# Kernel optimization log

Measured on AMD Instinct MI355X. Metric: run time of the kernel, lower is better.

Reference implementation:

```python
import jax, jax.numpy as jnp
import numpy as np

K_CHUNK = 512  # key-chunk size used by the module when n > 5000


def setup_inputs() -> dict:
    key = jax.random.key(0)
    ks = jax.random.split(key, 9)
    b, n, d = 1, 8192, 512
    s = 1.0 / np.sqrt(d)
    x = jax.random.normal(ks[0], (b, n, d), dtype=jnp.float32)
    Wq = jax.random.normal(ks[1], (d, d), dtype=jnp.float32) * s
    bq = jax.random.normal(ks[2], (d,), dtype=jnp.float32) * 0.01
    Wk = jax.random.normal(ks[3], (d, d), dtype=jnp.float32) * s
    bk = jax.random.normal(ks[4], (d,), dtype=jnp.float32) * 0.01
    Wv = jax.random.normal(ks[5], (d, d), dtype=jnp.float32) * s
    bv = jax.random.normal(ks[6], (d,), dtype=jnp.float32) * 0.01
    Wo = jax.random.normal(ks[7], (d, d), dtype=jnp.float32) * s
    bo = jax.random.normal(ks[8], (d,), dtype=jnp.float32) * 0.01
    return {"x": x, "Wq": Wq, "bq": bq, "Wk": Wk, "bk": bk,
            "Wv": Wv, "bv": bv, "Wo": Wo, "bo": bo}


def reference(x, Wq, bq, Wk, bk, Wv, bv, Wo, bo):
    # Faithful to the n > 5000 branch of SimpleAttenLayer (eval mode: dropout = identity).
    # The q-chunking in the original does not change the math (each q row is independent),
    # so we vectorize over all queries. The k-chunking DOES change the math: softmax is
    # applied within each 512-wide key block, then a second softmax over the concatenated
    # per-block weights, then matmul with full v.
    b, n, d = x.shape
    assert n % K_CHUNK == 0
    q = x @ Wq + bq
    k = x @ Wk + bk
    v = x @ Wv + bv
    scores = jnp.einsum('bnd,bmd->bnm', q, k) / jnp.sqrt(jnp.float32(d))
    # softmax within each key chunk of size K_CHUNK
    w1 = jax.nn.softmax(scores.reshape(b, n, n // K_CHUNK, K_CHUNK), axis=-1)
    w1 = w1.reshape(b, n, n)
    # second (global) softmax over the concatenated chunk weights
    w2 = jax.nn.softmax(w1, axis=-1)
    attn_out = jnp.einsum('bnm,bmd->bnd', w2, v)
    cls_attn_weights = w2[:, 0:1, :]  # [b, 1, n]
    out = x + (attn_out @ Wo + bo)
    return (out, cls_attn_weights)
```

## Files before the change

### kernel.cpp

```cpp
#include <hip/hip_runtime.h>
#include <stdint.h>

typedef unsigned short u16;
typedef uint8_t u8;
typedef __bf16 bf16x8 __attribute__((ext_vector_type(8)));
typedef float f32x4 __attribute__((ext_vector_type(4)));
typedef long i64x2 __attribute__((ext_vector_type(2)));

#define NTOK 8192
#define DD 512
#define CHK 512
#define NCH 16
#define LOG2E 1.4426950408889634f
#define SCL 0.044194173824159216f
#define SCLL 0.063762069130835270f

__device__ __forceinline__ u16 f2bf(float f) {
  union { float f; uint32_t u; } v; v.f = f;
  uint32_t r = v.u + 0x7FFFu + ((v.u >> 16) & 1u);
  return (u16)(r >> 16);
}

template <int CTRL>
__device__ __forceinline__ float dppadd(float x) {
  int y = __builtin_amdgcn_update_dpp(0, __float_as_int(x), CTRL, 0xF, 0xF, true);
  return x + __int_as_float(y);
}
__device__ __forceinline__ float rowsum16(float x) {
  x = dppadd<0xB1>(x);
  x = dppadd<0x4E>(x);
  x = dppadd<0x141>(x);
  x = dppadd<0x140>(x);
  return x;
}

typedef const __attribute__((address_space(1))) unsigned int* gas_t;
typedef __attribute__((address_space(3))) unsigned int* las_t;
__device__ __forceinline__ void gload16(const void* g, void* l) {
  __builtin_amdgcn_global_load_lds((gas_t)g, (las_t)l, 16, 0, 0);
}

__device__ __forceinline__ void vm4bar() {
  asm volatile("s_waitcnt vmcnt(4)\n\ts_barrier" ::: "memory");
}
__device__ __forceinline__ void vm2bar() {
  asm volatile("s_waitcnt vmcnt(2)\n\ts_barrier" ::: "memory");
}
__device__ __forceinline__ void vm0bar() {
  asm volatile("s_waitcnt vmcnt(0)\n\ts_barrier" ::: "memory");
}
__device__ __forceinline__ void barx() {
  asm volatile("s_barrier" ::: "memory");
}
__device__ __forceinline__ void lgkm0() {
  asm volatile("s_waitcnt lgkmcnt(0)" ::: "memory");
  __builtin_amdgcn_sched_barrier(0);
}

__device__ __forceinline__ int ilv64(int p) {
  const int g = p >> 3;
  return (((g & 3) * 2) + (g >> 2)) * 8 + (p & 7);
}
__device__ __forceinline__ int fperm(int t) {
  const int p = ((t & 15) << 2) | ((t >> 4) & 3);
  return (t & ~63) | ilv64(p);
}

__global__ void prep_kernel(const float* __restrict__ x, const float* __restrict__ Wq,
                            const float* __restrict__ Wk, const float* __restrict__ Wv,
                            const float* __restrict__ Wo, const float* __restrict__ bq,
                            u16* __restrict__ xb, u16* __restrict__ Wall, u16* __restrict__ WoT,
                            float* __restrict__ lsum, float* __restrict__ q0g) {
  __shared__ float t[32][33];
  const int bid = blockIdx.x;
  const int tid = threadIdx.x;
  if (bid < 4096) {
    int i = bid * 256 + tid;
    if (bid < 32) lsum[bid * 256 + tid] = 0.f;
    float4 v = ((const float4*)x)[i];
    ushort4 o;
    o.x = f2bf(v.x); o.y = f2bf(v.y); o.z = f2bf(v.z); o.w = f2bf(v.w);
    ((ushort4*)xb)[i] = o;
  } else if (bid < 5120) {
    const int tt = bid - 4096;
    const int z = tt >> 8, idx = tt & 255;
    const float* W; u16* WT;
    if (z == 0)      { W = Wq; WT = Wall; }
    else if (z == 1) { W = Wk; WT = Wall + 512 * 512; }
    else if (z == 2) { W = Wv; WT = Wall + 2 * 512 * 512; }
    else             { W = Wo; WT = WoT; }
    const int n0 = (idx & 15) * 32, k0 = (idx >> 4) * 32;
    const int tx = tid & 31, ty = tid >> 5;
    #pragma unroll
    for (int i = 0; i < 4; i++)
      t[ty + 8 * i][tx] = W[(k0 + ty + 8 * i) * DD + n0 + tx];
    __syncthreads();
    #pragma unroll
    for (int i = 0; i < 4; i++)
      WT[(n0 + ty + 8 * i) * DD + k0 + tx] = f2bf(t[tx][ty + 8 * i]);
  } else {
    const int c = (bid - 5120) * 256 + tid;
    float acc = bq[c];
    #pragma unroll 8
    for (int i = 0; i < 512; i++) acc += x[i] * Wq[i * 512 + c];
    q0g[c] = acc;
  }
}

__launch_bounds__(256, 3)
__global__ void qkv_kernel(const u16* __restrict__ A, const u16* __restrict__ Wall,
                           const float* __restrict__ bq, const float* __restrict__ bk,
                           const float* __restrict__ bv, u8* __restrict__ qb8,
                           u8* __restrict__ kb8, u8* __restrict__ vT8) {
  __shared__ __align__(16) u16 As[2][128 * 32];
  __shared__ __align__(16) u16 Bs[2][128 * 32];
  const int m0 = blockIdx.x * 128;
  const int n0g = blockIdx.y * 128;
  const int which = blockIdx.y >> 2;
  const int n0 = n0g & 511;
  const int tid = threadIdx.x;
  const int w = tid >> 6, lane = tid & 63, lm = lane & 15, quad = lane >> 4;
  const int wm = w & 1, wn = w >> 1;
  f32x4 acc[4][4] = {};
  const int soff = tid * 16;
  const int srow = soff >> 6;
  const int scol = soff & 63;
  const char* Ag = (const char*)A + ((size_t)(m0 + srow) * DD) * 2 + scol;
  const char* Bg = (const char*)Wall + ((size_t)(n0g + srow) * DD) * 2 + scol;
  char* Al = (char*)As + w * 1024;
  char* Bl = (char*)Bs + w * 1024;
  const size_t rs = (size_t)64 * DD * 2;

  auto stage = [&](int kk, int buf) {
    const char* ag = Ag + (size_t)kk * 2;
    const char* bg = Bg + (size_t)kk * 2;
    char* al = Al + buf * 8192;
    char* bl = Bl + buf * 8192;
    gload16(ag, al);
    gload16(ag + rs, al + 4096);
    gload16(bg, bl);
    gload16(bg + rs, bl + 4096);
  };

  stage(0, 0);
  for (int t = 0; t < 16; ++t) {
    const int cur = t & 1;
    if (t < 15) { stage((t + 1) * 32, cur ^ 1); vm4bar(); }
    else vm0bar();
    bf16x8 af[4], bfr[4];
    #pragma unroll
    for (int i = 0; i < 4; i++) af[i] = *(const bf16x8*)&As[cur][(wm * 64 + i * 16 + lm) * 32 + quad * 8];
    #pragma unroll
    for (int j = 0; j < 4; j++) bfr[j] = *(const bf16x8*)&Bs[cur][(wn * 64 + j * 16 + lm) * 32 + quad * 8];
    lgkm0();
    #pragma unroll
    for (int i = 0; i < 4; i++)
      #pragma unroll
      for (int j = 0; j < 4; j++)
        acc[i][j] = __builtin_amdgcn_mfma_f32_16x16x32_bf16(af[i], bfr[j], acc[i][j], 0, 0, 0);
    barx();
  }
  const float* bias = (which == 0) ? bq : (which == 1) ? bk : bv;
  #pragma unroll
  for (int i = 0; i < 4; i++) {
    const int row0 = m0 + wm * 64 + i * 16 + quad * 4;
    #pragma unroll
    for (int j = 0; j < 4; j++) {
      const int col = n0 + wn * 64 + j * 16 + lm;
      const float bv_ = bias[col];
      if (which == 2) {
        #pragma unroll
        for (int r = 0; r < 4; r++) {
          const float val = acc[i][j][r] + bv_;
          uint32_t pk = __builtin_amdgcn_cvt_pk_fp8_f32(val, val, 0, false);
          vT8[(size_t)col * NTOK + fperm(row0 + r)] = (u8)(pk & 0xFF);
        }
      } else {
        u8* dst = (which == 0) ? qb8 : kb8;
        const int icol = (col & ~63) | ilv64(col & 63);
        #pragma unroll
        for (int r = 0; r < 4; r++) {
          const float val = acc[i][j][r] + bv_;
          uint32_t pk = __builtin_amdgcn_cvt_pk_fp8_f32(val, val, 0, false);
          dst[(size_t)(row0 + r) * DD + icol] = (u8)(pk & 0xFF);
        }
      }
    }
  }
}

__launch_bounds__(256, 3)
__global__ void outproj_kernel(const u16* __restrict__ A, const u16* __restrict__ BT,
                               const float* __restrict__ bias, float* __restrict__ outp,
                               const float* __restrict__ resid) {
  __shared__ __align__(16) u16 As[2][128 * 32];
  __shared__ __align__(16) u16 Bs[2][128 * 32];
  const int m0 = blockIdx.x * 128, n0 = blockIdx.y * 128;
  const int tid = threadIdx.x;
  const int w = tid >> 6, lane = tid & 63, lm = lane & 15, quad = lane >> 4;
  const int wm = w & 1, wn = w >> 1;
  f32x4 acc[4][4] = {};
  const int soff = tid * 16;
  const int srow = soff >> 6;
  const int scol = soff & 63;
  const char* Ag = (const char*)A + ((size_t)(m0 + srow) * DD) * 2 + scol;
  const char* Bg = (const char*)BT + ((size_t)(n0 + srow) * DD) * 2 + scol;
  char* Al = (char*)As + w * 1024;
  char* Bl = (char*)Bs + w * 1024;
  const size_t rs = (size_t)64 * DD * 2;

  auto stage = [&](int kk, int buf) {
    const char* ag = Ag + (size_t)kk * 2;
    const char* bg = Bg + (size_t)kk * 2;
    char* al = Al + buf * 8192;
    char* bl = Bl + buf * 8192;
    gload16(ag, al);
    gload16(ag + rs, al + 4096);
    gload16(bg, bl);
    gload16(bg + rs, bl + 4096);
  };

  stage(0, 0);
  for (int t = 0; t < 16; ++t) {
    const int cur = t & 1;
    if (t < 15) { stage((t + 1) * 32, cur ^ 1); vm4bar(); }
    else vm0bar();
    bf16x8 af[4], bfr[4];
    #pragma unroll
    for (int i = 0; i < 4; i++) af[i] = *(const bf16x8*)&As[cur][(wm * 64 + i * 16 + lm) * 32 + quad * 8];
    #pragma unroll
    for (int j = 0; j < 4; j++) bfr[j] = *(const bf16x8*)&Bs[cur][(wn * 64 + j * 16 + lm) * 32 + quad * 8];
    lgkm0();
    #pragma unroll
    for (int i = 0; i < 4; i++)
      #pragma unroll
      for (int j = 0; j < 4; j++)
        acc[i][j] = __builtin_amdgcn_mfma_f32_16x16x32_bf16(af[i], bfr[j], acc[i][j], 0, 0, 0);
    barx();
  }
  #pragma unroll
  for (int i = 0; i < 4; i++) {
    const int row0 = m0 + wm * 64 + i * 16 + quad * 4;
    #pragma unroll
    for (int j = 0; j < 4; j++) {
      const int col = n0 + wn * 64 + j * 16 + lm;
      const float bv = bias[col];
      #pragma unroll
      for (int r = 0; r < 4; r++) {
        const size_t idx = (size_t)(row0 + r) * DD + col;
        outp[idx] = acc[i][j][r] + bv + resid[idx];
      }
    }
  }
}

__launch_bounds__(512, 2)
__global__ void gemm_pv_kernel(const u8* __restrict__ A, const u8* __restrict__ BT,
                               const float* __restrict__ lsum, u16* __restrict__ attnb) {
  __shared__ __align__(16) u8 As[2][128 * 64];
  __shared__ __align__(16) u8 Bs[2][128 * 64];
  const int m0 = blockIdx.x * 128, n0 = blockIdx.y * 128;
  const int tid = threadIdx.x;
  const int w = tid >> 6, lane = tid & 63, lm = lane & 15, quad = lane >> 4;
  const int wm = w >> 1, wn = w & 1;
  f32x4 acc[2][4] = {};
  const int srow = tid >> 2;
  const int scol = ((tid & 3) ^ ((srow >> 1) & 3)) * 16;
  const u8* Ag = A + (size_t)(m0 + srow) * NTOK + scol;
  const u8* Bg = BT + (size_t)(n0 + srow) * NTOK + scol;
  u8* Al = (u8*)As + w * 1024;
  u8* Bl = (u8*)Bs + w * 1024;
  const int csel = ((quad ^ ((lm >> 1) & 3)) * 16);

  auto stage = [&](int kk, int buf) {
    gload16(Ag + kk, Al + buf * 8192);
    gload16(Bg + kk, Bl + buf * 8192);
  };

  stage(0, 0);
  int cur = 0;
  for (int kk = 0; kk < NTOK; kk += 64) {
    if (kk + 64 < NTOK) { stage(kk + 64, cur ^ 1); vm2bar(); }
    else vm0bar();
    i64x2 afv[2], bfv[4];
    #pragma unroll
    for (int i = 0; i < 2; i++)
      afv[i] = *(const i64x2*)&As[cur][(wm * 32 + i * 16 + lm) * 64 + csel];
    #pragma unroll
    for (int j = 0; j < 4; j++)
      bfv[j] = *(const i64x2*)&Bs[cur][(wn * 64 + j * 16 + lm) * 64 + csel];
    lgkm0();
    #pragma unroll
    for (int i = 0; i < 2; i++)
      #pragma unroll
      for (int j = 0; j < 4; j++) {
        acc[i][j] = __builtin_amdgcn_mfma_f32_16x16x32_fp8_fp8(afv[i].x, bfv[j].x, acc[i][j], 0, 0, 0);
        acc[i][j] = __builtin_amdgcn_mfma_f32_16x16x32_fp8_fp8(afv[i].y, bfv[j].y, acc[i][j], 0, 0, 0);
      }
    barx();
    cur ^= 1;
  }
  #pragma unroll
  for (int i = 0; i < 2; i++) {
    const int row0 = m0 + wm * 32 + i * 16 + quad * 4;
    float li[4];
    #pragma unroll
    for (int r = 0; r < 4; r++) li[r] = 1.0f / lsum[row0 + r];
    #pragma unroll
    for (int j = 0; j < 4; j++) {
      const int col = n0 + wn * 64 + j * 16 + lm;
      #pragma unroll
      for (int r = 0; r < 4; r++)
        attnb[(size_t)(row0 + r) * DD + col] = f2bf(acc[i][j][r] * li[r]);
    }
  }
}

__launch_bounds__(512, 4)
__global__ void scores_kernel(const u8* __restrict__ qb8, const u8* __restrict__ kb8,
                              u8* __restrict__ P8, float* __restrict__ lsum) {
  __shared__ __align__(16) u8 As[2][64 * 64];
  __shared__ __align__(16) u8 Bs[2][512 * 64];
  __shared__ float hS[8][64], hP[8][64], hZ[64];
  const int m0 = blockIdx.x * 64;
  const int c = blockIdx.y;
  const int tid = threadIdx.x;
  const int w = tid >> 6, lane = tid & 63, lm = lane & 15, quad = lane >> 4;
  const int wsl = w;
  f32x4 s[4][4] = {};
  const int srA = tid >> 2;
  const int scS = ((tid & 3) ^ ((srA >> 1) & 3)) * 16;
  const u8* Qg = qb8 + (size_t)(m0 + srA) * DD + scS;
  const u8* Kg = kb8 + (size_t)(c * CHK + srA) * DD + scS;
  u8* Al = (u8*)As + w * 1024;
  u8* Bl = (u8*)Bs + w * 1024;
  const int csel = ((quad ^ ((lm >> 1) & 3)) * 16);

  auto stage = [&](int kk, int buf) {
    u8* al = Al + buf * 4096;
    u8* bl = Bl + buf * 32768;
    if (tid < 256) gload16(Qg + kk, al);
    gload16(Kg + kk, bl);
    gload16(Kg + kk + (size_t)128 * DD, bl + 8192);
    gload16(Kg + kk + (size_t)256 * DD, bl + 16384);
    gload16(Kg + kk + (size_t)384 * DD, bl + 24576);
  };

  stage(0, 0);
  vm0bar();
  #pragma unroll
  for (int t = 0; t < 8; ++t) {
    const int cur = t & 1;
    if (t < 7) stage((t + 1) * 64, cur ^ 1);
    i64x2 afv[4], bfv[4];
    #pragma unroll
    for (int i = 0; i < 4; i++)
      afv[i] = *(const i64x2*)&As[cur][(i * 16 + lm) * 64 + csel];
    #pragma unroll
    for (int j = 0; j < 4; j++)
      bfv[j] = *(const i64x2*)&Bs[cur][(wsl * 64 + j * 16 + lm) * 64 + csel];
    lgkm0();
    __builtin_amdgcn_s_setprio(1);
    #pragma unroll
    for (int i = 0; i < 4; i++)
      #pragma unroll
      for (int j = 0; j < 4; j++) {
        s[i][j] = __builtin_amdgcn_mfma_f32_16x16x32_fp8_fp8(afv[i].x, bfv[j].x, s[i][j], 0, 0, 0);
        s[i][j] = __builtin_amdgcn_mfma_f32_16x16x32_fp8_fp8(afv[i].y, bfv[j].y, s[i][j], 0, 0, 0);
      }
    __builtin_amdgcn_s_setprio(0);
    vm0bar();
  }
  #pragma unroll
  for (int i = 0; i < 4; i++) {
    #pragma unroll
    for (int reg = 0; reg < 4; reg++) {
      float z = 0.f;
      #pragma unroll
      for (int j = 0; j < 4; j++) {
        float e = exp2f(s[i][j][reg] * SCLL);
        s[i][j][reg] = e;
        z += e;
      }
      z = rowsum16(z);
      if (lm == 0) hS[wsl][i * 16 + quad * 4 + reg] = z;
    }
  }
  __syncthreads();
  if (tid < 64) {
    float t = 0.f;
    #pragma unroll
    for (int w2 = 0; w2 < 8; w2++) t += hS[w2][tid];
    hZ[tid] = LOG2E / t;
  }
  __syncthreads();
  const int newc = ((lm >> 1) & 3) * 2 + (lm >> 3);
  const int pbyte = wsl * 64 + newc * 8 + (lm & 1) * 4;
  #pragma unroll
  for (int i = 0; i < 4; i++) {
    #pragma unroll
    for (int reg = 0; reg < 4; reg++) {
      const int rl = i * 16 + quad * 4 + reg;
      const float iz = hZ[rl];
      const float p0 = exp2f(s[i][0][reg] * iz);
      const float p1 = exp2f(s[i][1][reg] * iz);
      const float p2 = exp2f(s[i][2][reg] * iz);
      const float p3 = exp2f(s[i][3][reg] * iz);
      float zp = (p0 + p1) + (p2 + p3);
      zp = rowsum16(zp);
      if (lm == 0) hP[wsl][rl] = zp;
      uint32_t o = __builtin_amdgcn_cvt_pk_fp8_f32(p0, p1, 0, false);
      o = __builtin_amdgcn_cvt_pk_fp8_f32(p2, p3, o, true);
      *(uint32_t*)(P8 + (size_t)(m0 + rl) * NTOK + c * CHK + pbyte) = o;
    }
  }
  __syncthreads();
  if (tid < 64) {
    float t = 0.f;
    #pragma unroll
    for (int w2 = 0; w2 < 8; w2++) t += hP[w2][tid];
    atomicAdd(&lsum[m0 + tid], t);
  }
}

__global__ void cls_u_kernel(const float* __restrict__ Wk, const float* __restrict__ bk,
                             const float* __restrict__ q0g, float* __restrict__ uc) {
  __shared__ float q0[512];
  const int tid = threadIdx.x;
  q0[tid] = q0g[tid];
  q0[tid + 256] = q0g[tid + 256];
  __syncthreads();
  if (blockIdx.x < 8) {
    const int c = blockIdx.x * 64 + (tid >> 2), ii = tid & 3;
    float acc = 0.f;
    #pragma unroll 8
    for (int j = ii; j < 512; j += 4) acc += Wk[(size_t)c * 512 + j] * q0[j];
    acc += __shfl_xor(acc, 1, 64);
    acc += __shfl_xor(acc, 2, 64);
    if (ii == 0) uc[c] = acc;
  } else if (tid < 64) {
    float acc = 0.f;
    #pragma unroll 8
    for (int j = tid; j < 512; j += 64) acc += bk[j] * q0[j];
    #pragma unroll
    for (int off = 1; off < 64; off <<= 1) acc += __shfl_xor(acc, off, 64);
    if (tid == 0) uc[512] = acc;
  }
}

__global__ void cls_scores_kernel(const float* __restrict__ x, const float* __restrict__ uc,
                                  float* __restrict__ s0) {
  __shared__ float u[512];
  __shared__ float c0s;
  int tid = threadIdx.x;
  for (int i = tid; i < 512; i += 256) u[i] = uc[i];
  if (tid == 0) c0s = uc[512];
  __syncthreads();
  int rowg = blockIdx.x * 32 + (tid >> 3);
  int ii = tid & 7;
  const float* xr = x + rowg * 512;
  float acc = 0.f;
  for (int i = ii; i < 512; i += 8) acc += xr[i] * u[i];
  acc += __shfl_xor(acc, 1, 64);
  acc += __shfl_xor(acc, 2, 64);
  acc += __shfl_xor(acc, 4, 64);
  if (ii == 0) s0[rowg] = (acc + c0s) * SCL;
}

__global__ void cls_softmax_kernel(const float* __restrict__ s0, float* __restrict__ out) {
  int tid = threadIdx.x;
  int w = tid >> 6, lane = tid & 63;
  const float* sc = s0 + w * 512;
  float v[8];
  float m = -1e30f;
  #pragma unroll
  for (int j = 0; j < 8; j++) { v[j] = sc[lane * 8 + j]; m = fmaxf(m, v[j]); }
  for (int off = 1; off < 64; off <<= 1) m = fmaxf(m, __shfl_xor(m, off, 64));
  float z = 0.f;
  #pragma unroll
  for (int j = 0; j < 8; j++) { v[j] = expf(v[j] - m); z += v[j]; }
  for (int off = 1; off < 64; off <<= 1) z += __shfl_xor(z, off, 64);
  float invz = 1.f / z;
  float l = 0.f;
  #pragma unroll
  for (int j = 0; j < 8; j++) { v[j] = expf(v[j] * invz); l += v[j]; }
  for (int off = 1; off < 64; off <<= 1) l += __shfl_xor(l, off, 64);
  __shared__ float lw[16];
  if (lane == 0) lw[w] = l;
  __syncthreads();
  float L = 0.f;
  for (int i = 0; i < 16; i++) L += lw[i];
  float invL = 1.f / L;
  #pragma unroll
  for (int j = 0; j < 8; j++) out[w * 512 + lane * 8 + j] = v[j] * invL;
}

extern "C" void kernel_launch(void* const* d_in, const int* in_sizes, int n_in,
                              void* d_out, int out_size, void* d_ws, size_t ws_size,
                              hipStream_t stream) {
  const float* x  = (const float*)d_in[0];
  const float* Wq = (const float*)d_in[1];
  const float* bq = (const float*)d_in[2];
  const float* Wk = (const float*)d_in[3];
  const float* bk = (const float*)d_in[4];
  const float* Wv = (const float*)d_in[5];
  const float* bv = (const float*)d_in[6];
  const float* Wo = (const float*)d_in[7];
  const float* bo = (const float*)d_in[8];
  float* out = (float*)d_out;

  char* ws = (char*)d_ws;
  u16* xb    = (u16*)(ws);
  u16* Wall  = (u16*)(ws + 8388608);
  u16* WoT   = (u16*)(ws + 9961472);
  u8*  qb8   = (u8*)(ws + 10485760);
  u8*  kb8   = (u8*)(ws + 14680064);
  u8*  vT8   = (u8*)(ws + 18874368);
  u16* attnb = (u16*)(ws + 23068672);
  float* q0g = (float*)(ws + 31457280);
  float* uc  = (float*)(ws + 31461376);
  float* s0  = (float*)(ws + 31465472);
  float* lsum= (float*)(ws + 31498240);
  u8*  P8    = (u8*)(ws + 31531008);

  prep_kernel<<<5122, 256, 0, stream>>>(x, Wq, Wk, Wv, Wo, bq, xb, Wall, WoT, lsum, q0g);

  qkv_kernel<<<dim3(NTOK / 128, 12), 256, 0, stream>>>(xb, Wall, bq, bk, bv, qb8, kb8, vT8);

  scores_kernel<<<dim3(NTOK / 64, NCH), 512, 0, stream>>>(qb8, kb8, P8, lsum);

  gemm_pv_kernel<<<dim3(NTOK / 128, DD / 128), 512, 0, stream>>>(P8, vT8, lsum, attnb);

  outproj_kernel<<<dim3(NTOK / 128, DD / 128), 256, 0, stream>>>(attnb, WoT, bo, out, x);

  cls_u_kernel<<<9, 256, 0, stream>>>(Wk, bk, q0g, uc);
  cls_scores_kernel<<<NTOK / 32, 256, 0, stream>>>(x, uc, s0);
  cls_softmax_kernel<<<1, 1024, 0, stream>>>(s0, out + (size_t)NTOK * DD);
}
```

Before: 318.5 us.

## Fuse scores softmax and PV GEMM into flash-style kernel with split-K partials

Merges the scores kernel and the PV GEMM into one kernel. Each block keeps a 64-row Q tile in LDS, computes the per-chunk double softmax for 8 key chunks, writes the FP8 probabilities to LDS instead of the 128 MB global P matrix, and immediately multiplies them by V. The key range is split across 2 blocks, each writing fp32 partial outputs, which a new reduce kernel sums, normalizes by lsum and converts to bf16. This removes the global round trip of the probability matrix. In exchange it adds larger LDS use (lower occupancy), serialized softmax and PV phases per chunk, and extra fp32 partial traffic.

```diff
diff --git a/kernel.cpp b/kernel.cpp
--- a/kernel.cpp
+++ b/kernel.cpp
@@ -10,7 +10,8 @@
 #define NTOK 8192
 #define DD 512
 #define CHK 512
-#define NCH 16
+#define CG 2
+#define CPB 8
 #define LOG2E 1.4426950408889634f
 #define SCL 0.044194173824159216f
 #define SCLL 0.063762069130835270f
@@ -43,9 +44,6 @@
 __device__ __forceinline__ void vm4bar() {
   asm volatile("s_waitcnt vmcnt(4)\n\ts_barrier" ::: "memory");
 }
-__device__ __forceinline__ void vm2bar() {
-  asm volatile("s_waitcnt vmcnt(2)\n\ts_barrier" ::: "memory");
-}
 __device__ __forceinline__ void vm0bar() {
   asm volatile("s_waitcnt vmcnt(0)\n\ts_barrier" ::: "memory");
 }
@@ -55,6 +53,9 @@
 __device__ __forceinline__ void lgkm0() {
   asm volatile("s_waitcnt lgkmcnt(0)" ::: "memory");
   __builtin_amdgcn_sched_barrier(0);
+}
+__device__ __forceinline__ void ldsbar() {
+  asm volatile("s_waitcnt lgkmcnt(0)\n\ts_barrier" ::: "memory");
 }
 
 __device__ __forceinline__ int ilv64(int p) {
@@ -255,172 +256,187 @@
 }
 
 __launch_bounds__(512, 2)
-__global__ void gemm_pv_kernel(const u8* __restrict__ A, const u8* __restrict__ BT,
-                               const float* __restrict__ lsum, u16* __restrict__ attnb) {
-  __shared__ __align__(16) u8 As[2][128 * 64];
-  __shared__ __align__(16) u8 Bs[2][128 * 64];
-  const int m0 = blockIdx.x * 128, n0 = blockIdx.y * 128;
-  const int tid = threadIdx.x;
-  const int w = tid >> 6, lane = tid & 63, lm = lane & 15, quad = lane >> 4;
-  const int wm = w >> 1, wn = w & 1;
-  f32x4 acc[2][4] = {};
-  const int srow = tid >> 2;
-  const int scol = ((tid & 3) ^ ((srow >> 1) & 3)) * 16;
-  const u8* Ag = A + (size_t)(m0 + srow) * NTOK + scol;
-  const u8* Bg = BT + (size_t)(n0 + srow) * NTOK + scol;
-  u8* Al = (u8*)As + w * 1024;
-  u8* Bl = (u8*)Bs + w * 1024;
-  const int csel = ((quad ^ ((lm >> 1) & 3)) * 16);
-
-  auto stage = [&](int kk, int buf) {
-    gload16(Ag + kk, Al + buf * 8192);
-    gload16(Bg + kk, Bl + buf * 8192);
-  };
-
-  stage(0, 0);
-  int cur = 0;
-  for (int kk = 0; kk < NTOK; kk += 64) {
-    if (kk + 64 < NTOK) { stage(kk + 64, cur ^ 1); vm2bar(); }
-    else vm0bar();
-    i64x2 afv[2], bfv[4];
-    #pragma unroll
-    for (int i = 0; i < 2; i++)
-      afv[i] = *(const i64x2*)&As[cur][(wm * 32 + i * 16 + lm) * 64 + csel];
-    #pragma unroll
-    for (int j = 0; j < 4; j++)
-      bfv[j] = *(const i64x2*)&Bs[cur][(wn * 64 + j * 16 + lm) * 64 + csel];
-    lgkm0();
-    #pragma unroll
-    for (int i = 0; i < 2; i++)
-      #pragma unroll
-      for (int j = 0; j < 4; j++) {
-        acc[i][j] = __builtin_amdgcn_mfma_f32_16x16x32_fp8_fp8(afv[i].x, bfv[j].x, acc[i][j], 0, 0, 0);
-        acc[i][j] = __builtin_amdgcn_mfma_f32_16x16x32_fp8_fp8(afv[i].y, bfv[j].y, acc[i][j], 0, 0, 0);
-      }
-    barx();
-    cur ^= 1;
-  }
-  #pragma unroll
-  for (int i = 0; i < 2; i++) {
-    const int row0 = m0 + wm * 32 + i * 16 + quad * 4;
-    float li[4];
-    #pragma unroll
-    for (int r = 0; r < 4; r++) li[r] = 1.0f / lsum[row0 + r];
-    #pragma unroll
-    for (int j = 0; j < 4; j++) {
-      const int col = n0 + wn * 64 + j * 16 + lm;
-      #pragma unroll
-      for (int r = 0; r < 4; r++)
-        attnb[(size_t)(row0 + r) * DD + col] = f2bf(acc[i][j][r] * li[r]);
-    }
-  }
-}
-
-__launch_bounds__(512, 4)
-__global__ void scores_kernel(const u8* __restrict__ qb8, const u8* __restrict__ kb8,
-                              u8* __restrict__ P8, float* __restrict__ lsum) {
-  __shared__ __align__(16) u8 As[2][64 * 64];
+__global__ void fused_attn_kernel(const u8* __restrict__ qb8, const u8* __restrict__ kb8,
+                                  const u8* __restrict__ vT8, float* __restrict__ part,
+                                  float* __restrict__ lsum) {
+  __shared__ __align__(16) u8 Qs[8 * 64 * 64];
   __shared__ __align__(16) u8 Bs[2][512 * 64];
+  __shared__ __align__(16) u8 Pl[64][528];
   __shared__ float hS[8][64], hP[8][64], hZ[64];
   const int m0 = blockIdx.x * 64;
-  const int c = blockIdx.y;
+  const int cg = blockIdx.y;
   const int tid = threadIdx.x;
   const int w = tid >> 6, lane = tid & 63, lm = lane & 15, quad = lane >> 4;
   const int wsl = w;
-  f32x4 s[4][4] = {};
+  f32x4 acc[4][4] = {};
   const int srA = tid >> 2;
   const int scS = ((tid & 3) ^ ((srA >> 1) & 3)) * 16;
-  const u8* Qg = qb8 + (size_t)(m0 + srA) * DD + scS;
-  const u8* Kg = kb8 + (size_t)(c * CHK + srA) * DD + scS;
-  u8* Al = (u8*)As + w * 1024;
+  const u8* Qg = qb8 + (size_t)(m0 + (srA & 63)) * DD + scS;
+  const u8* Kg = kb8 + ((size_t)cg * CPB * CHK + srA) * DD + scS;
+  const u8* Vg = vT8 + (size_t)srA * NTOK + (size_t)cg * CPB * CHK + scS;
   u8* Bl = (u8*)Bs + w * 1024;
   const int csel = ((quad ^ ((lm >> 1) & 3)) * 16);
 
-  auto stage = [&](int kk, int buf) {
-    u8* al = Al + buf * 4096;
+  auto stageK = [&](int c, int kk, int buf) {
     u8* bl = Bl + buf * 32768;
-    if (tid < 256) gload16(Qg + kk, al);
-    gload16(Kg + kk, bl);
-    gload16(Kg + kk + (size_t)128 * DD, bl + 8192);
-    gload16(Kg + kk + (size_t)256 * DD, bl + 16384);
-    gload16(Kg + kk + (size_t)384 * DD, bl + 24576);
+    const u8* kg = Kg + (size_t)c * CHK * DD + kk * 64;
+    gload16(kg, bl);
+    gload16(kg + (size_t)128 * DD, bl + 8192);
+    gload16(kg + (size_t)256 * DD, bl + 16384);
+    gload16(kg + (size_t)384 * DD, bl + 24576);
   };
-
-  stage(0, 0);
-  vm0bar();
-  #pragma unroll
-  for (int t = 0; t < 8; ++t) {
-    const int cur = t & 1;
-    if (t < 7) stage((t + 1) * 64, cur ^ 1);
-    i64x2 afv[4], bfv[4];
-    #pragma unroll
-    for (int i = 0; i < 4; i++)
-      afv[i] = *(const i64x2*)&As[cur][(i * 16 + lm) * 64 + csel];
-    #pragma unroll
-    for (int j = 0; j < 4; j++)
-      bfv[j] = *(const i64x2*)&Bs[cur][(wsl * 64 + j * 16 + lm) * 64 + csel];
-    lgkm0();
-    __builtin_amdgcn_s_setprio(1);
-    #pragma unroll
-    for (int i = 0; i < 4; i++)
-      #pragma unroll
-      for (int j = 0; j < 4; j++) {
-        s[i][j] = __builtin_amdgcn_mfma_f32_16x16x32_fp8_fp8(afv[i].x, bfv[j].x, s[i][j], 0, 0, 0);
-        s[i][j] = __builtin_amdgcn_mfma_f32_16x16x32_fp8_fp8(afv[i].y, bfv[j].y, s[i][j], 0, 0, 0);
-      }
-    __builtin_amdgcn_s_setprio(0);
-    vm0bar();
-  }
-  #pragma unroll
-  for (int i = 0; i < 4; i++) {
-    #pragma unroll
-    for (int reg = 0; reg < 4; reg++) {
-      float z = 0.f;
-      #pragma unroll
-      for (int j = 0; j < 4; j++) {
-        float e = exp2f(s[i][j][reg] * SCLL);
-        s[i][j][reg] = e;
-        z += e;
-      }
-      z = rowsum16(z);
-      if (lm == 0) hS[wsl][i * 16 + quad * 4 + reg] = z;
-    }
-  }
-  __syncthreads();
-  if (tid < 64) {
-    float t = 0.f;
-    #pragma unroll
-    for (int w2 = 0; w2 < 8; w2++) t += hS[w2][tid];
-    hZ[tid] = LOG2E / t;
-  }
-  __syncthreads();
+  auto stageV = [&](int c, int ks, int buf) {
+    u8* bl = Bl + buf * 32768;
+    const u8* vg = Vg + c * CHK + ks * 64;
+    gload16(vg, bl);
+    gload16(vg + (size_t)128 * NTOK, bl + 8192);
+    gload16(vg + (size_t)256 * NTOK, bl + 16384);
+    gload16(vg + (size_t)384 * NTOK, bl + 24576);
+  };
+
+  if (tid < 256) {
+    #pragma unroll
+    for (int kd = 0; kd < 8; kd++)
+      gload16(Qg + kd * 64, Qs + kd * 4096 + w * 1024);
+  }
+
+  float lrow = 0.f;
   const int newc = ((lm >> 1) & 3) * 2 + (lm >> 3);
   const int pbyte = wsl * 64 + newc * 8 + (lm & 1) * 4;
+
+  for (int c = 0; c < CPB; ++c) {
+    f32x4 s[4][4] = {};
+    stageK(c, 0, 0);
+    vm0bar();
+    #pragma unroll
+    for (int t = 0; t < 8; ++t) {
+      const int cur = t & 1;
+      if (t < 7) stageK(c, t + 1, cur ^ 1);
+      else stageV(c, 0, 0);
+      i64x2 afv[4], bfv[4];
+      #pragma unroll
+      for (int i = 0; i < 4; i++)
+        afv[i] = *(const i64x2*)&Qs[t * 4096 + (i * 16 + lm) * 64 + csel];
+      #pragma unroll
+      for (int j = 0; j < 4; j++)
+        bfv[j] = *(const i64x2*)&Bs[cur][(wsl * 64 + j * 16 + lm) * 64 + csel];
+      lgkm0();
+      __builtin_amdgcn_s_setprio(1);
+      #pragma unroll
+      for (int i = 0; i < 4; i++)
+        #pragma unroll
+        for (int j = 0; j < 4; j++) {
+          s[i][j] = __builtin_amdgcn_mfma_f32_16x16x32_fp8_fp8(afv[i].x, bfv[j].x, s[i][j], 0, 0, 0);
+          s[i][j] = __builtin_amdgcn_mfma_f32_16x16x32_fp8_fp8(afv[i].y, bfv[j].y, s[i][j], 0, 0, 0);
+        }
+      __builtin_amdgcn_s_setprio(0);
+      if (t < 7) vm0bar();
+    }
+    #pragma unroll
+    for (int i = 0; i < 4; i++) {
+      #pragma unroll
+      for (int reg = 0; reg < 4; reg++) {
+        float z = 0.f;
+        #pragma unroll
+        for (int j = 0; j < 4; j++) {
+          float e = exp2f(s[i][j][reg] * SCLL);
+          s[i][j][reg] = e;
+          z += e;
+        }
+        z = rowsum16(z);
+        if (lm == 0) hS[wsl][i * 16 + quad * 4 + reg] = z;
+      }
+    }
+    ldsbar();
+    if (tid < 64) {
+      float t = 0.f;
+      #pragma unroll
+      for (int w2 = 0; w2 < 8; w2++) t += hS[w2][tid];
+      hZ[tid] = LOG2E / t;
+    }
+    ldsbar();
+    #pragma unroll
+    for (int i = 0; i < 4; i++) {
+      #pragma unroll
+      for (int reg = 0; reg < 4; reg++) {
+        const int rl = i * 16 + quad * 4 + reg;
+        const float iz = hZ[rl];
+        const float p0 = exp2f(s[i][0][reg] * iz);
+        const float p1 = exp2f(s[i][1][reg] * iz);
+        const float p2 = exp2f(s[i][2][reg] * iz);
+        const float p3 = exp2f(s[i][3][reg] * iz);
+        float zp = (p0 + p1) + (p2 + p3);
+        zp = rowsum16(zp);
+        if (lm == 0) hP[wsl][rl] = zp;
+        uint32_t o = __builtin_amdgcn_cvt_pk_fp8_f32(p0, p1, 0, false);
+        o = __builtin_amdgcn_cvt_pk_fp8_f32(p2, p3, o, true);
+        *(uint32_t*)&Pl[rl][pbyte] = o;
+      }
+    }
+    ldsbar();
+    if (tid < 64) {
+      float t = 0.f;
+      #pragma unroll
+      for (int w2 = 0; w2 < 8; w2++) t += hP[w2][tid];
+      lrow += t;
+    }
+    vm0bar();
+    #pragma unroll
+    for (int t = 0; t < 8; ++t) {
+      const int cur = t & 1;
+      if (t < 7) stageV(c, t + 1, cur ^ 1);
+      i64x2 afv[4], bfv[4];
+      #pragma unroll
+      for (int i = 0; i < 4; i++)
+        afv[i] = *(const i64x2*)&Pl[i * 16 + lm][t * 64 + quad * 16];
+      #pragma unroll
+      for (int j = 0; j < 4; j++)
+        bfv[j] = *(const i64x2*)&Bs[cur][(wsl * 64 + j * 16 + lm) * 64 + csel];
+      lgkm0();
+      __builtin_amdgcn_s_setprio(1);
+      #pragma unroll
+      for (int i = 0; i < 4; i++)
+        #pragma unroll
+        for (int j = 0; j < 4; j++) {
+          acc[i][j] = __builtin_amdgcn_mfma_f32_16x16x32_fp8_fp8(afv[i].x, bfv[j].x, acc[i][j], 0, 0, 0);
+          acc[i][j] = __builtin_amdgcn_mfma_f32_16x16x32_fp8_fp8(afv[i].y, bfv[j].y, acc[i][j], 0, 0, 0);
+        }
+      __builtin_amdgcn_s_setprio(0);
+      if (t < 7) vm0bar();
+      else barx();
+    }
+  }
+  if (tid < 64) atomicAdd(&lsum[m0 + tid], lrow);
+  float* po = part + (size_t)cg * NTOK * DD;
   #pragma unroll
   for (int i = 0; i < 4; i++) {
-    #pragma unroll
-    for (int reg = 0; reg < 4; reg++) {
-      const int rl = i * 16 + quad * 4 + reg;
-      const float iz = hZ[rl];
-      const float p0 = exp2f(s[i][0][reg] * iz);
-      const float p1 = exp2f(s[i][1][reg] * iz);
-      const float p2 = exp2f(s[i][2][reg] * iz);
-      const float p3 = exp2f(s[i][3][reg] * iz);
-      float zp = (p0 + p1) + (p2 + p3);
-      zp = rowsum16(zp);
-      if (lm == 0) hP[wsl][rl] = zp;
-      uint32_t o = __builtin_amdgcn_cvt_pk_fp8_f32(p0, p1, 0, false);
-      o = __builtin_amdgcn_cvt_pk_fp8_f32(p2, p3, o, true);
-      *(uint32_t*)(P8 + (size_t)(m0 + rl) * NTOK + c * CHK + pbyte) = o;
-    }
-  }
-  __syncthreads();
-  if (tid < 64) {
-    float t = 0.f;
-    #pragma unroll
-    for (int w2 = 0; w2 < 8; w2++) t += hP[w2][tid];
-    atomicAdd(&lsum[m0 + tid], t);
-  }
+    const int row0 = m0 + i * 16 + quad * 4;
+    #pragma unroll
+    for (int j = 0; j < 4; j++) {
+      const int col = wsl * 64 + j * 16 + lm;
+      #pragma unroll
+      for (int r = 0; r < 4; r++)
+        po[(size_t)(row0 + r) * DD + col] = acc[i][j][r];
+    }
+  }
+}
+
+__global__ void pv_reduce_kernel(const float* __restrict__ part, const float* __restrict__ lsum,
+                                 u16* __restrict__ attnb) {
+  const int idx = blockIdx.x * 256 + threadIdx.x;
+  const int row = idx >> 7;
+  const int c4 = (idx & 127) << 2;
+  const float* p = part + (size_t)row * DD + c4;
+  const size_t stride = (size_t)NTOK * DD;
+  float4 a = *(const float4*)(p);
+  float4 b = *(const float4*)(p + stride);
+  const float inv = 1.0f / lsum[row];
+  ushort4 o;
+  o.x = f2bf((a.x + b.x) * inv);
+  o.y = f2bf((a.y + b.y) * inv);
+  o.z = f2bf((a.z + b.z) * inv);
+  o.w = f2bf((a.w + b.w) * inv);
+  *(ushort4*)(attnb + (size_t)row * DD + c4) = o;
 }
 
 __global__ void cls_u_kernel(const float* __restrict__ Wk, const float* __restrict__ bk,
@@ -521,15 +537,15 @@
   float* uc  = (float*)(ws + 31461376);
   float* s0  = (float*)(ws + 31465472);
   float* lsum= (float*)(ws + 31498240);
-  u8*  P8    = (u8*)(ws + 31531008);
+  float* part= (float*)(ws + 98639872);
 
   prep_kernel<<<5122, 256, 0, stream>>>(x, Wq, Wk, Wv, Wo, bq, xb, Wall, WoT, lsum, q0g);
 
   qkv_kernel<<<dim3(NTOK / 128, 12), 256, 0, stream>>>(xb, Wall, bq, bk, bv, qb8, kb8, vT8);
 
-  scores_kernel<<<dim3(NTOK / 64, NCH), 512, 0, stream>>>(qb8, kb8, P8, lsum);
-
-  gemm_pv_kernel<<<dim3(NTOK / 128, DD / 128), 512, 0, stream>>>(P8, vT8, lsum, attnb);
+  fused_attn_kernel<<<dim3(NTOK / 64, CG), 512, 0, stream>>>(qb8, kb8, vT8, part, lsum);
+
+  pv_reduce_kernel<<<NTOK * DD / 4 / 256, 256, 0, stream>>>(part, lsum, attnb);
 
   outproj_kernel<<<dim3(NTOK / 128, DD / 128), 256, 0, stream>>>(attnb, WoT, bo, out, x);
 
```

New measurement: 327.2 us. +2.7%, slower.
